# Kernel optimization log

Hardware: AMD Instinct MI355X
Metric: run time of the kernel (lower is better)

Reference implementation:

```python
import jax, jax.numpy as jnp
import numpy as np

N, E = 20000, 320000
IN_DIM, HID, OUT_DIM, HEADS = 128, 64, 64, 4


def _lin_params(key, fan_in, fan_out):
    kw, kb = jax.random.split(key)
    s = 1.0 / np.sqrt(fan_in)
    W = jax.random.uniform(kw, (fan_in, fan_out), jnp.float32, -s, s)
    b = jax.random.uniform(kb, (fan_out,), jnp.float32, -s, s)
    return W, b


def setup_inputs() -> dict:
    key = jax.random.key(0)
    ks = jax.random.split(key, 12)
    x = jax.random.normal(ks[0], (N, IN_DIM), jnp.float32)
    edge_index = jax.random.randint(ks[1], (2, E), 0, N, jnp.int64)
    W1, b1 = _lin_params(ks[2], IN_DIM, HID)
    # conv1: in=HID, per-head out=HID, heads=HEADS, concat=True
    Wq1, bq1 = _lin_params(ks[3], HID, HID * HEADS)
    Wk1, bk1 = _lin_params(ks[4], HID, HID * HEADS)
    Wv1, bv1 = _lin_params(ks[5], HID, HID * HEADS)
    Ws1, bs1 = _lin_params(ks[6], HID, HID * HEADS)
    # conv2: in=HID*HEADS, out=OUT_DIM, heads=1, concat=False
    Wq2, bq2 = _lin_params(ks[7], HID * HEADS, OUT_DIM)
    Wk2, bk2 = _lin_params(ks[8], HID * HEADS, OUT_DIM)
    Wv2, bv2 = _lin_params(ks[9], HID * HEADS, OUT_DIM)
    Ws2, bs2 = _lin_params(ks[10], HID * HEADS, OUT_DIM)
    return dict(x=x, edge_index=edge_index, W1=W1, b1=b1,
                Wq1=Wq1, bq1=bq1, Wk1=Wk1, bk1=bk1, Wv1=Wv1, bv1=bv1, Ws1=Ws1, bs1=bs1,
                Wq2=Wq2, bq2=bq2, Wk2=Wk2, bk2=bk2, Wv2=Wv2, bv2=bv2, Ws2=Ws2, bs2=bs2)


def transformer_conv(x, src, dst, Wq, bq, Wk, bk, Wv, bv, Ws, bs, heads, concat):
    n = x.shape[0]
    c = Wq.shape[1] // heads  # per-head channels
    q = (x @ Wq + bq).reshape(n, heads, c)
    k = (x @ Wk + bk).reshape(n, heads, c)
    v = (x @ Wv + bv).reshape(n, heads, c)
    # per-edge attention logits, grouped-by-dst softmax
    alpha = jnp.einsum('ehc,ehc->eh', q[dst], k[src]) / jnp.sqrt(jnp.float32(c))
    m = jax.ops.segment_max(alpha, dst, num_segments=n)  # [n, heads]
    m = jnp.where(jnp.isfinite(m), m, 0.0)
    ex = jnp.exp(alpha - m[dst])
    denom = jax.ops.segment_sum(ex, dst, num_segments=n)
    a = ex / (denom[dst] + 1e-16)  # [E, heads]
    out = jax.ops.segment_sum(a[..., None] * v[src], dst, num_segments=n)  # [n, heads, c]
    out = out.reshape(n, heads * c) if concat else out.mean(axis=1)
    return out + (x @ Ws + bs)  # root/skip connection


def reference(x, edge_index, W1, b1, Wq1, bq1, Wk1, bk1, Wv1, bv1, Ws1, bs1,
              Wq2, bq2, Wk2, bk2, Wv2, bv2, Ws2, bs2):
    src, dst = edge_index[0], edge_index[1]
    h = jax.nn.relu(x @ W1 + b1)
    h = transformer_conv(h, src, dst, Wq1, bq1, Wk1, bk1, Wv1, bv1, Ws1, bs1, HEADS, True)
    h = jax.nn.relu(h)  # dropout is identity in eval mode
    out = transformer_conv(h, src, dst, Wq2, bq2, Wk2, bk2, Wv2, bv2, Ws2, bs2, 1, False)
    return out
```

## Files before the change

### kernel.cpp

```cpp
#include <hip/hip_runtime.h>
#include <hip/hip_bf16.h>
#include <math.h>

typedef short short8 __attribute__((ext_vector_type(8)));
typedef float f32x4 __attribute__((ext_vector_type(4)));
typedef float f32x2 __attribute__((ext_vector_type(2)));

__device__ __forceinline__ unsigned short pk_bf16(float x) {
    unsigned int b = __float_as_uint(x);
    b += 0x7fffu + ((b >> 16) & 1u);
    return (unsigned short)(b >> 16);
}
__device__ __forceinline__ void unpack8(const uint4 u, float* f) {
    f[0] = __uint_as_float(u.x << 16); f[1] = __uint_as_float(u.x & 0xffff0000u);
    f[2] = __uint_as_float(u.y << 16); f[3] = __uint_as_float(u.y & 0xffff0000u);
    f[4] = __uint_as_float(u.z << 16); f[5] = __uint_as_float(u.z & 0xffff0000u);
    f[6] = __uint_as_float(u.w << 16); f[7] = __uint_as_float(u.w & 0xffff0000u);
}
__device__ __forceinline__ unsigned char enc_fp8(float x) {
    return (unsigned char)(__builtin_amdgcn_cvt_pk_fp8_f32(x, x, 0, false) & 0xff);
}
__device__ __forceinline__ void unpack8_fp8(const uint2 u, float* f) {
    f32x2 a = __builtin_amdgcn_cvt_pk_f32_fp8(u.x, false);
    f32x2 b = __builtin_amdgcn_cvt_pk_f32_fp8(u.x, true);
    f32x2 c = __builtin_amdgcn_cvt_pk_f32_fp8(u.y, false);
    f32x2 d = __builtin_amdgcn_cvt_pk_f32_fp8(u.y, true);
    f[0] = a.x; f[1] = a.y; f[2] = b.x; f[3] = b.y;
    f[4] = c.x; f[5] = c.y; f[6] = d.x; f[7] = d.y;
}
__device__ __forceinline__ float qsum4(float x) {
    x += __int_as_float(__builtin_amdgcn_mov_dpp(__float_as_int(x), 0xB1, 0xF, 0xF, true));
    x += __int_as_float(__builtin_amdgcn_mov_dpp(__float_as_int(x), 0x4E, 0xF, 0xF, true));
    return x;
}

__global__ void count_kernel(const int* __restrict__ dst, int* __restrict__ deg, int E) {
    int e = blockIdx.x * blockDim.x + threadIdx.x;
    if (e < E) atomicAdd(&deg[dst[e]], 1);
}

__global__ __launch_bounds__(1024) void scan_kernel(const int* __restrict__ deg,
                                                    int* __restrict__ offs,
                                                    int* __restrict__ cursor,
                                                    int n, int nb) {
    __shared__ int s[1024];
    const int b = blockIdx.x, t = threadIdx.x;
    int partial = 0;
    for (int i = t; i < b * 1024; i += 1024) partial += deg[i];
    s[t] = partial;
    __syncthreads();
    for (int off = 512; off > 0; off >>= 1) {
        if (t < off) s[t] += s[t + off];
        __syncthreads();
    }
    const int base = s[0];
    __syncthreads();
    const int i = b * 1024 + t;
    const int v = (i < n) ? deg[i] : 0;
    s[t] = v;
    __syncthreads();
    for (int off = 1; off < 1024; off <<= 1) {
        int x = (t >= off) ? s[t - off] : 0;
        __syncthreads();
        s[t] += x;
        __syncthreads();
    }
    if (i < n) {
        const int o = base + s[t] - v;
        offs[i] = o;
        cursor[i] = o;
    }
    if (b == nb - 1 && t == 1023) offs[n] = base + s[1023];
}

template <int K, int NT, int CFG>
__device__ __forceinline__ void convw_body(const float* Wa, const float* Wb,
                                           const float* Wc, const float* Wd,
                                           unsigned short* out, int t) {
    constexpr int KS = K / 32;
    if (t >= NT * K * 64) return;
    const int jj = t & 7;
    const int lane = (t >> 3) & 63;
    const int nf = (t >> 9) & 3;
    const int rest = t >> 11;
    const int ks = rest % KS;
    const int nt = rest / KS;
    const int k = ks * 32 + (lane >> 4) * 8 + jj;
    const int c64 = nf * 16 + (lane & 15);
    float v;
    if (CFG == 1) {
        const int j = nt >> 2;
        const float* W = (j == 0) ? Wa : (j == 1) ? Wb : (j == 2) ? Wc : Wd;
        v = W[(size_t)k * 256 + (nt & 3) * 64 + c64];
    } else if (CFG == 2) {
        const float* W = (nt == 0) ? Wa : (nt == 1) ? Wb : (nt == 2) ? Wc : Wd;
        v = W[(size_t)k * 64 + c64];
    } else {
        v = Wa[(size_t)k * 64 + c64];
    }
    out[t] = pk_bf16(v);
}

__global__ __launch_bounds__(256) void prep_kernel(
    const float* __restrict__ x, unsigned short* __restrict__ xb, int nx, int nA,
    const float* __restrict__ W1, unsigned short* __restrict__ wswzL,
    const float* __restrict__ Wq1, const float* __restrict__ Wk1,
    const float* __restrict__ Wv1, const float* __restrict__ Ws1,
    unsigned short* __restrict__ wswz1,
    const float* __restrict__ Wq2, const float* __restrict__ Wk2,
    const float* __restrict__ Wv2, const float* __restrict__ Ws2,
    unsigned short* __restrict__ wswz2,
    int* __restrict__ deg, int ndeg) {
    int b = blockIdx.x;
    if (b < nA) {
        int t = b * 256 + threadIdx.x;
        if (t < nx) xb[t] = pk_bf16(x[t]);
        return;
    }
    b -= nA;
    if (b < 32) { convw_body<128, 1, 0>(W1, W1, W1, W1, wswzL, b * 256 + threadIdx.x); return; }
    b -= 32;
    if (b < 256) { convw_body<64, 16, 1>(Wq1, Wk1, Wv1, Ws1, wswz1, b * 256 + threadIdx.x); return; }
    b -= 256;
    if (b < 256) { convw_body<256, 4, 2>(Wq2, Wk2, Wv2, Ws2, wswz2, b * 256 + threadIdx.x); return; }
    b -= 256;
    {
        int t = b * 256 + threadIdx.x;
        if (t < ndeg) deg[t] = 0;
    }
}

template <int K, int NT, int KIND>
__global__ __launch_bounds__(256) void mfma_gemm_kernel(
    const unsigned short* __restrict__ A, const unsigned short* __restrict__ Wswz,
    const float* __restrict__ ba, const float* __restrict__ bb,
    const float* __restrict__ bc, const float* __restrict__ bd,
    unsigned short* __restrict__ qout, unsigned char* __restrict__ kvout,
    void* __restrict__ sout, int n) {
    constexpr int KS = K / 32;
    const int nt = blockIdx.x;
    const int w = threadIdx.x >> 6, l = threadIdx.x & 63;
    const int r0 = blockIdx.y * 64 + w * 16;
    const int lrow = l & 15, lk = l >> 4;

    f32x4 acc[4] = {};
    const unsigned short* wp = Wswz + (size_t)nt * KS * 4 * 512 + (size_t)l * 8;
    const unsigned short* ap = A + (size_t)(r0 + lrow) * K + lk * 8;

#pragma unroll
    for (int ks = 0; ks < KS; ++ks) {
        const short8 a = *(const short8*)(ap + ks * 32);
        const short8 b0 = *(const short8*)(wp + (ks * 4 + 0) * 512);
        const short8 b1 = *(const short8*)(wp + (ks * 4 + 1) * 512);
        const short8 b2 = *(const short8*)(wp + (ks * 4 + 2) * 512);
        const short8 b3 = *(const short8*)(wp + (ks * 4 + 3) * 512);
        acc[0] = __builtin_amdgcn_mfma_f32_16x16x32_bf16(a, b0, acc[0], 0, 0, 0);
        acc[1] = __builtin_amdgcn_mfma_f32_16x16x32_bf16(a, b1, acc[1], 0, 0, 0);
        acc[2] = __builtin_amdgcn_mfma_f32_16x16x32_bf16(a, b2, acc[2], 0, 0, 0);
        acc[3] = __builtin_amdgcn_mfma_f32_16x16x32_bf16(a, b3, acc[3], 0, 0, 0);
    }

    const int colg = l & 15, rowg = l >> 4;
#pragma unroll
    for (int nf = 0; nf < 4; ++nf) {
        const int c64 = nf * 16 + colg;
        float bias;
        if (KIND == 1) {
            const int j = nt >> 2;
            const float* bsel = (j == 0) ? ba : (j == 1) ? bb : (j == 2) ? bc : bd;
            bias = bsel[(nt & 3) * 64 + c64];
        } else {
            const float* bsel = (nt == 0) ? ba : (nt == 1) ? bb : (nt == 2) ? bc : bd;
            bias = bsel[c64];
        }
#pragma unroll
        for (int r = 0; r < 4; ++r) {
            const int row = r0 + rowg * 4 + r;
            if (row >= n) continue;
            const float val = acc[nf][r] + bias;
            if (KIND == 1) {
                const int j = nt >> 2, hd = nt & 3;
                if (j == 0) {
                    qout[(size_t)row * 256 + hd * 64 + c64] = pk_bf16(val);
                } else if (j == 1) {
                    kvout[((size_t)row * 4 + hd) * 192 + c64] = enc_fp8(val);
                } else if (j == 2) {
                    *(unsigned short*)(kvout + ((size_t)row * 4 + hd) * 192 + 64 + c64 * 2) =
                        pk_bf16(val);
                } else {
                    ((unsigned short*)sout)[(size_t)row * 256 + hd * 64 + c64] = pk_bf16(val);
                }
            } else {
                if (nt == 0) {
                    qout[(size_t)row * 64 + c64] = pk_bf16(val);
                } else if (nt == 1) {
                    kvout[(size_t)row * 192 + c64] = enc_fp8(val);
                } else if (nt == 2) {
                    *(unsigned short*)(kvout + (size_t)row * 192 + 64 + c64 * 2) = pk_bf16(val);
                } else {
                    ((float*)sout)[(size_t)row * 64 + c64] = val;
                }
            }
        }
    }
}

__device__ __forceinline__ void lin_body(const unsigned short* __restrict__ A,
                                         const unsigned short* __restrict__ Wswz,
                                         const float* __restrict__ bias,
                                         unsigned short* __restrict__ hout,
                                         int n, int by, int tid) {
    constexpr int K = 128, KS = 4;
    const int w = tid >> 6, l = tid & 63;
    const int r0 = by * 64 + w * 16;
    const int lrow = l & 15, lk = l >> 4;

    f32x4 acc[4] = {};
    const unsigned short* wp = Wswz + (size_t)l * 8;
    const unsigned short* ap = A + (size_t)(r0 + lrow) * K + lk * 8;

#pragma unroll
    for (int ks = 0; ks < KS; ++ks) {
        const short8 a = *(const short8*)(ap + ks * 32);
        const short8 b0 = *(const short8*)(wp + (ks * 4 + 0) * 512);
        const short8 b1 = *(const short8*)(wp + (ks * 4 + 1) * 512);
        const short8 b2 = *(const short8*)(wp + (ks * 4 + 2) * 512);
        const short8 b3 = *(const short8*)(wp + (ks * 4 + 3) * 512);
        acc[0] = __builtin_amdgcn_mfma_f32_16x16x32_bf16(a, b0, acc[0], 0, 0, 0);
        acc[1] = __builtin_amdgcn_mfma_f32_16x16x32_bf16(a, b1, acc[1], 0, 0, 0);
        acc[2] = __builtin_amdgcn_mfma_f32_16x16x32_bf16(a, b2, acc[2], 0, 0, 0);
        acc[3] = __builtin_amdgcn_mfma_f32_16x16x32_bf16(a, b3, acc[3], 0, 0, 0);
    }
    const int colg = l & 15, rowg = l >> 4;
#pragma unroll
    for (int nf = 0; nf < 4; ++nf) {
        const int c64 = nf * 16 + colg;
        const float bias_v = bias[c64];
#pragma unroll
        for (int r = 0; r < 4; ++r) {
            const int row = r0 + rowg * 4 + r;
            if (row >= n) continue;
            hout[(size_t)row * 64 + c64] = pk_bf16(fmaxf(acc[nf][r] + bias_v, 0.f));
        }
    }
}

__global__ __launch_bounds__(256) void fill_lin_kernel(
    const int* __restrict__ src, const int* __restrict__ dst,
    int* __restrict__ cursor, int* __restrict__ csrc, int E, int nfill,
    const unsigned short* __restrict__ xb, const unsigned short* __restrict__ wswzL,
    const float* __restrict__ b1, unsigned short* __restrict__ h1b, int n) {
    if ((int)blockIdx.x < nfill) {
        int e = blockIdx.x * 256 + threadIdx.x;
        if (e < E) {
            int p = atomicAdd(&cursor[dst[e]], 1);
            csrc[p] = src[e];
        }
        return;
    }
    lin_body(xb, wswzL, b1, h1b, n, blockIdx.x - nfill, threadIdx.x);
}

__global__ __launch_bounds__(256) void attn4_kernel(
    const unsigned short* __restrict__ q, const unsigned char* __restrict__ kv,
    const unsigned short* __restrict__ s,
    const int* __restrict__ offs, const int* __restrict__ csrc,
    unsigned short* __restrict__ out, int n) {
    const int bid = blockIdx.x;
    const int head = (bid & 7) >> 1;
    const int ng = (bid >> 3) * 2 + (bid & 1);
    const int lane = threadIdx.x & 63;
    const int node = ng * 4 + (threadIdx.x >> 6);
    if (node >= n) return;
    const int g = lane >> 3;
    const int sl = lane & 7;
    const unsigned colbase = (head << 6) + (sl << 3);
    const unsigned koff = head * 192 + sl * 8;
    const unsigned voff = head * 192 + 64 + sl * 16;

    float qv[8];
    {
        uint4 qu = *(const uint4*)(q + ((unsigned)node << 8) + colbase);
        unpack8(qu, qv);
        const float qs = 0.125f * 1.44269504f;
#pragma unroll
        for (int i = 0; i < 8; ++i) qv[i] *= qs;
    }

    const int e0 = offs[node], e1 = offs[node + 1];
    float denom = 0.f;
    float acc[8] = {0.f, 0.f, 0.f, 0.f, 0.f, 0.f, 0.f, 0.f};

    int e = e0 + g;
    bool valid = e < e1;
    uint2 ku; uint4 vu;
    if (valid) {
        const unsigned char* kvp = kv + (size_t)(unsigned)csrc[e] * 768;
        ku = *(const uint2*)(kvp + koff);
        vu = *(const uint4*)(kvp + voff);
    }
    int en = e + 8;
    bool vn = en < e1;
    int srcn = vn ? csrc[en] : 0;

    while (valid) {
        uint2 kun; uint4 vun;
        if (vn) {
            const unsigned char* kvp = kv + (size_t)(unsigned)srcn * 768;
            kun = *(const uint2*)(kvp + koff);
            vun = *(const uint4*)(kvp + voff);
        }
        const int en2 = en + 8;
        const bool vn2 = en2 < e1;
        const int srcn2 = vn2 ? csrc[en2] : 0;

        float kf[8], vf[8];
        unpack8_fp8(ku, kf); unpack8(vu, vf);
        float dot = qv[0] * kf[0] + qv[1] * kf[1] + qv[2] * kf[2] + qv[3] * kf[3]
                  + qv[4] * kf[4] + qv[5] * kf[5] + qv[6] * kf[6] + qv[7] * kf[7];
        dot = qsum4(dot);
        dot += __shfl_xor(dot, 4, 64);
        const float wgt = __builtin_amdgcn_exp2f(dot);
#pragma unroll
        for (int i = 0; i < 8; ++i) acc[i] = fmaf(wgt, vf[i], acc[i]);
        denom += wgt;

        valid = vn; vn = vn2;
        en = en2; srcn = srcn2;
        ku = kun; vu = vun;
    }

#pragma unroll
    for (int off = 8; off <= 32; off <<= 1) {
        denom += __shfl_xor(denom, off, 64);
#pragma unroll
        for (int i = 0; i < 8; ++i) acc[i] += __shfl_xor(acc[i], off, 64);
    }

    if (g == 0) {
        float sv[8];
        uint4 su = *(const uint4*)(s + ((unsigned)node << 8) + colbase);
        unpack8(su, sv);
        const float inv = 1.f / (denom + 1e-16f);
        uint4 p;
        unsigned r[8];
#pragma unroll
        for (int i = 0; i < 8; ++i) r[i] = pk_bf16(fmaxf(acc[i] * inv + sv[i], 0.f));
        p.x = r[0] | (r[1] << 16);
        p.y = r[2] | (r[3] << 16);
        p.z = r[4] | (r[5] << 16);
        p.w = r[6] | (r[7] << 16);
        *(uint4*)(out + ((unsigned)node << 8) + colbase) = p;
    }
}

__global__ __launch_bounds__(256) void attn1_kernel(
    const unsigned short* __restrict__ q, const unsigned char* __restrict__ kv,
    const float* __restrict__ s,
    const int* __restrict__ offs, const int* __restrict__ csrc,
    float* __restrict__ out, int n) {
    const int w = threadIdx.x >> 6;
    const int lane = threadIdx.x & 63;
    const int g = lane >> 3;
    const int sl = lane & 7;
    const int node = blockIdx.x * 4 + w;
    if (node >= n) return;
    const unsigned koff = sl * 8;
    const unsigned voff = 64 + sl * 16;

    float qv[8];
    {
        uint4 qu = *(const uint4*)(q + ((unsigned)node << 6) + (sl << 3));
        unpack8(qu, qv);
        const float qs = 0.125f * 1.44269504f;
#pragma unroll
        for (int i = 0; i < 8; ++i) qv[i] *= qs;
    }

    const int e0 = offs[node], e1 = offs[node + 1];
    float denom = 0.f;
    float acc[8] = {0.f, 0.f, 0.f, 0.f, 0.f, 0.f, 0.f, 0.f};

    int e = e0 + g;
    bool valid = e < e1;
    uint2 ku; uint4 vu;
    if (valid) {
        const unsigned char* kvp = kv + (size_t)(unsigned)csrc[e] * 192;
        ku = *(const uint2*)(kvp + koff);
        vu = *(const uint4*)(kvp + voff);
    }
    int en = e + 8;
    bool vn = en < e1;
    int srcn = vn ? csrc[en] : 0;

    while (valid) {
        uint2 kun; uint4 vun;
        if (vn) {
            const unsigned char* kvp = kv + (size_t)(unsigned)srcn * 192;
            kun = *(const uint2*)(kvp + koff);
            vun = *(const uint4*)(kvp + voff);
        }
        const int en2 = en + 8;
        const bool vn2 = en2 < e1;
        const int srcn2 = vn2 ? csrc[en2] : 0;

        float kf[8], vf[8];
        unpack8_fp8(ku, kf); unpack8(vu, vf);
        float dot = qv[0] * kf[0] + qv[1] * kf[1] + qv[2] * kf[2] + qv[3] * kf[3]
                  + qv[4] * kf[4] + qv[5] * kf[5] + qv[6] * kf[6] + qv[7] * kf[7];
        dot = qsum4(dot);
        dot += __shfl_xor(dot, 4, 64);
        const float wgt = __builtin_amdgcn_exp2f(dot);
#pragma unroll
        for (int i = 0; i < 8; ++i) acc[i] = fmaf(wgt, vf[i], acc[i]);
        denom += wgt;

        valid = vn; vn = vn2;
        en = en2; srcn = srcn2;
        ku = kun; vu = vun;
    }

#pragma unroll
    for (int off = 8; off <= 32; off <<= 1) {
        denom += __shfl_xor(denom, off, 64);
#pragma unroll
        for (int i = 0; i < 8; ++i) acc[i] += __shfl_xor(acc[i], off, 64);
    }

    if (g == 0) {
        const float* sp = s + ((unsigned)node << 6) + (sl << 3);
        const float4 sva = *(const float4*)sp;
        const float4 svb = *(const float4*)(sp + 4);
        const float inv = 1.f / (denom + 1e-16f);
        float4 oa, ob;
        oa.x = acc[0] * inv + sva.x; oa.y = acc[1] * inv + sva.y;
        oa.z = acc[2] * inv + sva.z; oa.w = acc[3] * inv + sva.w;
        ob.x = acc[4] * inv + svb.x; ob.y = acc[5] * inv + svb.y;
        ob.z = acc[6] * inv + svb.z; ob.w = acc[7] * inv + svb.w;
        float* op = out + ((unsigned)node << 6) + (sl << 3);
        *(float4*)op = oa;
        *(float4*)(op + 4) = ob;
    }
}

extern "C" void kernel_launch(void* const* d_in, const int* in_sizes, int n_in,
                              void* d_out, int out_size, void* d_ws, size_t ws_size,
                              hipStream_t stream) {
    const float* x   = (const float*)d_in[0];
    const int*   ei  = (const int*)d_in[1];
    const float* W1  = (const float*)d_in[2];
    const float* b1  = (const float*)d_in[3];
    const float* Wq1 = (const float*)d_in[4];  const float* bq1 = (const float*)d_in[5];
    const float* Wk1 = (const float*)d_in[6];  const float* bk1 = (const float*)d_in[7];
    const float* Wv1 = (const float*)d_in[8];  const float* bv1 = (const float*)d_in[9];
    const float* Ws1 = (const float*)d_in[10]; const float* bs1 = (const float*)d_in[11];
    const float* Wq2 = (const float*)d_in[12]; const float* bq2 = (const float*)d_in[13];
    const float* Wk2 = (const float*)d_in[14]; const float* bk2 = (const float*)d_in[15];
    const float* Wv2 = (const float*)d_in[16]; const float* bv2 = (const float*)d_in[17];
    const float* Ws2 = (const float*)d_in[18]; const float* bs2 = (const float*)d_in[19];

    const int N = in_sizes[0] / 128;
    const int E = in_sizes[1] / 2;
    const int* srcv = ei;
    const int* dstv = ei + E;
    const int rowgroups = (N + 63) / 64;
    const int Mpad = rowgroups * 64;
    const int nscan = (N + 1023) / 1024;

    char* p = (char*)d_ws;
    auto alloc = [&](size_t bytes) -> void* {
        void* r = (void*)p;
        p += (bytes + 255) & ~(size_t)255;
        return r;
    };
    unsigned short* xb  = (unsigned short*)alloc((size_t)Mpad * 128 * 2);
    unsigned short* h1b = (unsigned short*)alloc((size_t)Mpad * 64 * 2);
    unsigned short* q1b = (unsigned short*)alloc((size_t)N * 256 * 2);
    unsigned char*  kv1 = (unsigned char*)alloc((size_t)N * 4 * 192);
    unsigned short* s1b = (unsigned short*)alloc((size_t)N * 256 * 2);
    unsigned short* h2b = (unsigned short*)alloc((size_t)Mpad * 256 * 2);
    unsigned short* q2b = (unsigned short*)alloc((size_t)N * 64 * 2);
    unsigned char*  kv2 = (unsigned char*)alloc((size_t)N * 192);
    float* s2 = (float*)alloc((size_t)N * 64 * 4);
    unsigned short* wswzL = (unsigned short*)alloc((size_t)1 * 128 * 64 * 2);
    unsigned short* wswz1 = (unsigned short*)alloc((size_t)16 * 64 * 64 * 2);
    unsigned short* wswz2 = (unsigned short*)alloc((size_t)4 * 256 * 64 * 2);
    int* deg    = (int*)alloc((size_t)N * 4);
    int* offs   = (int*)alloc(((size_t)N + 1) * 4);
    int* cursor = (int*)alloc((size_t)N * 4);
    int* csrc   = (int*)alloc((size_t)E * 4);
    (void)ws_size; (void)n_in; (void)out_size;

    const int nx = N * 128;
    const int nA = (nx + 255) / 256;
    const int nZ = (N + 255) / 256;
    prep_kernel<<<nA + 32 + 256 + 256 + nZ, 256, 0, stream>>>(
        x, xb, nx, nA, W1, wswzL, Wq1, Wk1, Wv1, Ws1, wswz1,
        Wq2, Wk2, Wv2, Ws2, wswz2, deg, N);

    count_kernel<<<(E + 255) / 256, 256, 0, stream>>>(dstv, deg, E);

    scan_kernel<<<nscan, 1024, 0, stream>>>(deg, offs, cursor, N, nscan);

    const int nfill = (E + 255) / 256;
    fill_lin_kernel<<<nfill + rowgroups, 256, 0, stream>>>(
        srcv, dstv, cursor, csrc, E, nfill, xb, wswzL, b1, h1b, N);

    mfma_gemm_kernel<64, 16, 1><<<dim3(16, rowgroups), 256, 0, stream>>>(
        h1b, wswz1, bq1, bk1, bv1, bs1, q1b, kv1, (void*)s1b, N);

    const int ngroups = (N + 3) / 4;
    const int npairs = (ngroups + 1) / 2;
    attn4_kernel<<<npairs * 8, 256, 0, stream>>>(q1b, kv1, s1b, offs, csrc, h2b, N);

    mfma_gemm_kernel<256, 4, 2><<<dim3(4, rowgroups), 256, 0, stream>>>(
        h2b, wswz2, bq2, bk2, bv2, bs2, q2b, kv2, (void*)s2, N);

    attn1_kernel<<<(N + 3) / 4, 256, 0, stream>>>(q2b, kv2, s2, offs, csrc,
                                                  (float*)d_out, N);
}
```

Baseline: 147.8 us.

## Store layer-1 V in fp8 and interleave K/V head-major for single gathers

Layer-1 values drop from bf16 to fp8 and are interleaved with keys in one 128-byte row per (head, node), stored head-major so each head's gather touches a compact array. Each attention lane now issues one 16-byte load per edge instead of an 8-byte and a 16-byte load. This cuts gather traffic and the size of the kv buffer. V loses precision (fp8), which adds error to the attention output.

```diff
diff --git a/kernel.cpp b/kernel.cpp
--- a/kernel.cpp
+++ b/kernel.cpp
@@ -27,6 +27,20 @@
     f32x2 d = __builtin_amdgcn_cvt_pk_f32_fp8(u.y, true);
     f[0] = a.x; f[1] = a.y; f[2] = b.x; f[3] = b.y;
     f[4] = c.x; f[5] = c.y; f[6] = d.x; f[7] = d.y;
+}
+__device__ __forceinline__ void unpack_kv8(const uint4 u, float* k, float* v) {
+    f32x2 a0 = __builtin_amdgcn_cvt_pk_f32_fp8(u.x, false);
+    f32x2 a1 = __builtin_amdgcn_cvt_pk_f32_fp8(u.x, true);
+    f32x2 b0 = __builtin_amdgcn_cvt_pk_f32_fp8(u.y, false);
+    f32x2 b1 = __builtin_amdgcn_cvt_pk_f32_fp8(u.y, true);
+    f32x2 c0 = __builtin_amdgcn_cvt_pk_f32_fp8(u.z, false);
+    f32x2 c1 = __builtin_amdgcn_cvt_pk_f32_fp8(u.z, true);
+    f32x2 d0 = __builtin_amdgcn_cvt_pk_f32_fp8(u.w, false);
+    f32x2 d1 = __builtin_amdgcn_cvt_pk_f32_fp8(u.w, true);
+    k[0] = a0.x; v[0] = a0.y; k[1] = a1.x; v[1] = a1.y;
+    k[2] = b0.x; v[2] = b0.y; k[3] = b1.x; v[3] = b1.y;
+    k[4] = c0.x; v[4] = c0.y; k[5] = c1.x; v[5] = c1.y;
+    k[6] = d0.x; v[6] = d0.y; k[7] = d1.x; v[7] = d1.y;
 }
 __device__ __forceinline__ float qsum4(float x) {
     x += __int_as_float(__builtin_amdgcn_mov_dpp(__float_as_int(x), 0xB1, 0xF, 0xF, true));
@@ -183,10 +197,9 @@
                 if (j == 0) {
                     qout[(size_t)row * 256 + hd * 64 + c64] = pk_bf16(val);
                 } else if (j == 1) {
-                    kvout[((size_t)row * 4 + hd) * 192 + c64] = enc_fp8(val);
+                    kvout[((size_t)hd * n + row) * 128 + c64 * 2] = enc_fp8(val);
                 } else if (j == 2) {
-                    *(unsigned short*)(kvout + ((size_t)row * 4 + hd) * 192 + 64 + c64 * 2) =
-                        pk_bf16(val);
+                    kvout[((size_t)hd * n + row) * 128 + c64 * 2 + 1] = enc_fp8(val);
                 } else {
                     ((unsigned short*)sout)[(size_t)row * 256 + hd * 64 + c64] = pk_bf16(val);
                 }
@@ -275,8 +288,7 @@
     const int g = lane >> 3;
     const int sl = lane & 7;
     const unsigned colbase = (head << 6) + (sl << 3);
-    const unsigned koff = head * 192 + sl * 8;
-    const unsigned voff = head * 192 + 64 + sl * 16;
+    const unsigned char* kvlane = kv + ((size_t)head * n) * 128 + sl * 16;
 
     float qv[8];
     {
@@ -293,29 +305,21 @@
 
     int e = e0 + g;
     bool valid = e < e1;
-    uint2 ku; uint4 vu;
-    if (valid) {
-        const unsigned char* kvp = kv + (size_t)(unsigned)csrc[e] * 768;
-        ku = *(const uint2*)(kvp + koff);
-        vu = *(const uint4*)(kvp + voff);
-    }
+    uint4 uu;
+    if (valid) uu = *(const uint4*)(kvlane + ((unsigned)csrc[e] << 7));
     int en = e + 8;
     bool vn = en < e1;
     int srcn = vn ? csrc[en] : 0;
 
     while (valid) {
-        uint2 kun; uint4 vun;
-        if (vn) {
-            const unsigned char* kvp = kv + (size_t)(unsigned)srcn * 768;
-            kun = *(const uint2*)(kvp + koff);
-            vun = *(const uint4*)(kvp + voff);
-        }
+        uint4 uun;
+        if (vn) uun = *(const uint4*)(kvlane + ((unsigned)srcn << 7));
         const int en2 = en + 8;
         const bool vn2 = en2 < e1;
         const int srcn2 = vn2 ? csrc[en2] : 0;
 
         float kf[8], vf[8];
-        unpack8_fp8(ku, kf); unpack8(vu, vf);
+        unpack_kv8(uu, kf, vf);
         float dot = qv[0] * kf[0] + qv[1] * kf[1] + qv[2] * kf[2] + qv[3] * kf[3]
                   + qv[4] * kf[4] + qv[5] * kf[5] + qv[6] * kf[6] + qv[7] * kf[7];
         dot = qsum4(dot);
@@ -327,7 +331,7 @@
 
         valid = vn; vn = vn2;
         en = en2; srcn = srcn2;
-        ku = kun; vu = vun;
+        uu = uun;
     }
 
 #pragma unroll
@@ -476,7 +480,7 @@
     unsigned short* xb  = (unsigned short*)alloc((size_t)Mpad * 128 * 2);
     unsigned short* h1b = (unsigned short*)alloc((size_t)Mpad * 64 * 2);
     unsigned short* q1b = (unsigned short*)alloc((size_t)N * 256 * 2);
-    unsigned char*  kv1 = (unsigned char*)alloc((size_t)N * 4 * 192);
+    unsigned char*  kv1 = (unsigned char*)alloc((size_t)N * 4 * 128);
     unsigned short* s1b = (unsigned short*)alloc((size_t)N * 256 * 2);
     unsigned short* h2b = (unsigned short*)alloc((size_t)Mpad * 256 * 2);
     unsigned short* q2b = (unsigned short*)alloc((size_t)N * 64 * 2);
```

Result: no change. 145.6 us (-1.5%).
